# Optimization experiments

Measured on AMD Instinct MI355X. Metric: run time of the kernel, lower is better.

Reference implementation:

```python
import jax, jax.numpy as jnp
import numpy as np

K = 9            # connections per output pixel
GA = 2           # global additional samples
RA = 2           # relative additional samples
VS = 4 + GA + RA # 2^rank neighbours + sampled
REGION = 12      # int(0.25 * 48) per spatial dim
MMULT = 0.1
MIN_SIGMA = 0.05
SIGMA_SCALE = 0.05
SIGMA_BOOST = 2.0


def setup_inputs() -> dict:
    key = jax.random.key(0)
    ks = jax.random.split(key, 8)
    b, cin, h, w = 8, 128, 48, 48
    cout = 256
    hidden = cin * 4

    def lin_init(k, fan_out, fan_in):
        bound = 1.0 / np.sqrt(fan_in)
        kw, kb = jax.random.split(k)
        W = jax.random.uniform(kw, (fan_out, fan_in), minval=-bound, maxval=bound, dtype=jnp.float32)
        bb = jax.random.uniform(kb, (fan_out,), minval=-bound, maxval=bound, dtype=jnp.float32)
        return W, bb

    x = jax.random.normal(ks[0], (b, cin, h, w), dtype=jnp.float32)
    W1, b1 = lin_init(ks[1], hidden, 2)          # toparams layer 1 (adaptive=False -> 2 coord inputs)
    W2, b2 = lin_init(ks[2], 3 * K, hidden)      # toparams layer 2 -> k means (2d) + k sigmas
    Wu, bu = lin_init(ks[3], cout, K * cin)      # unify linear
    gints = jax.random.randint(ks[4], (b, h, w, K, GA, 2), 0, h, dtype=jnp.int32)      # global samples (h==w)
    roff = jax.random.randint(ks[5], (b, h, w, K, RA, 2), 0, REGION, dtype=jnp.int32)  # relative offsets
    return {"x": x, "W1": W1, "b1": b1, "W2": W2, "b2": b2, "Wu": Wu, "bu": bu,
            "gints": gints, "roff": roff}


def reference(x, W1, b1, W2, b2, Wu, bu, gints, roff):
    b, c, h, w = x.shape
    s = jnp.array([h, w], dtype=x.dtype)                       # spatial range per dim
    s_int = jnp.array([h, w], dtype=jnp.int32)

    # normalized coordinate grid in [0,1], (h, w, 2) with [.,.,0]=row, [.,.,1]=col
    rows = jnp.arange(h, dtype=x.dtype) / (h - 1)
    cols = jnp.arange(w, dtype=x.dtype) / (w - 1)
    coords = jnp.stack(jnp.meshgrid(rows, cols, indexing='ij'), axis=-1)

    # hypernetwork: per-pixel coords -> K 2d mean offsets + K sigmas
    inp = jnp.broadcast_to(coords, (b, h, w, 2))
    hid = jax.nn.relu(inp @ W1.T + b1)
    params = hid @ W2.T + b2                                   # (b,h,w,3K)
    means_raw = params[..., :2 * K].reshape(b, h, w, K, 2)
    sig_raw = params[..., 2 * K:]                              # (b,h,w,K)

    # mids: inverse of the sigmoid scaling applied to the pixel's own coordinate
    pix = coords * (s - 1)                                     # pixel coordinates
    sc = pix / (s - 1) * 0.9999 + 0.00005
    mids = jnp.log(sc / (1.0 - sc))                            # (h,w,2)

    # transform_means: sigmoid -> [0, s-1]
    means = jax.nn.sigmoid(mids[None, :, :, None, :] + MMULT * means_raw) * (s - 1)  # (b,h,w,K,2)
    # transform_sigmas: softplus(. + boost) + min, per-dim scale, then sigma_scale
    sigmas = (jax.nn.softplus(sig_raw + SIGMA_BOOST) + MIN_SIGMA)[..., None] * s * SIGMA_SCALE  # (b,h,w,K,2)

    # ---- integer index generation (non-differentiable) ----
    fl = jnp.floor(jax.lax.stop_gradient(means)).astype(jnp.int32)   # (b,h,w,K,2)
    combos = jnp.array([[0, 0], [0, 1], [1, 0], [1, 1]], dtype=jnp.int32)
    neigh = fl[..., None, :] + combos                                 # (b,h,w,K,4,2)
    rel = fl[..., None, :] + roff - REGION // 2                       # (b,h,w,K,RA,2)
    ints = jnp.concatenate([neigh, gints, rel], axis=-2) % s_int      # (b,h,w,K,VS,2)

    # duplicate masking: zero any tuple that occurred earlier along VS
    eq = jnp.all(ints[..., :, None, :] == ints[..., None, :, :], axis=-1)  # (...,VS,VS)
    lower = jnp.tril(jnp.ones((VS, VS), dtype=bool), k=-1)
    dups = jnp.any(eq & lower, axis=-1)                               # (b,h,w,K,VS)

    # unnormalized gaussian densities of integer points under (means, sigmas)
    diff = (ints.astype(x.dtype) - means[..., None, :]) / sigmas[..., None, :]
    props = jnp.exp(-0.5 * jnp.sum(diff * diff, axis=-1))             # (b,h,w,K,VS)
    props = jnp.where(dups, jnp.zeros((), x.dtype), props)
    weights = props / jnp.sum(props, axis=-1, keepdims=True)          # mvalues are all-ones

    # irregular gather of input channel vectors at sampled pixels
    lin = ints[..., 0] * w + ints[..., 1]                             # (b,h,w,K,VS)
    flat = x.transpose(0, 2, 3, 1).reshape(b, h * w, c)
    feats = flat[jnp.arange(b)[:, None], lin.reshape(b, -1)]          # (b, h*w*K*VS, c)
    feats = feats.reshape(b, h, w, K, VS, c)

    feats = jnp.einsum('bhwkvc,bhwkv->bhwkc', feats, weights)         # weighted reduce over VS
    feats = feats.reshape(b, h, w, K * c)
    out = feats @ Wu.T + bu                                           # unify linear
    return out.transpose(0, 3, 1, 2)                                  # (b, cout, h, w)
```

## Files before the change

### kernel.cpp

```cpp
#include <hip/hip_runtime.h>
#include <hip/hip_bf16.h>
#include <hip/hip_fp16.h>

#define BB 8
#define CIN 128
#define HH 48
#define WW 48
#define HW 2304
#define KK 9
#define COUT 256
#define KC 1152
#define MM 18432
#define MT 16
#define SFP 136

#define LIGHT_BARRIER() asm volatile("s_waitcnt lgkmcnt(0)\n\ts_barrier" ::: "memory")

typedef short bf16x8_t __attribute__((ext_vector_type(8)));
typedef float f32x4_t  __attribute__((ext_vector_type(4)));

static __device__ __forceinline__ float b2f(short u) {
    union { unsigned int i; float f; } c;
    c.i = ((unsigned int)(unsigned short)u) << 16;
    return c.f;
}

__global__ __launch_bounds__(256) void prep_kernel(
    const float* __restrict__ x, __hip_bfloat16* __restrict__ xT,
    const float* __restrict__ Wu, bf16x8_t* __restrict__ Bp,
    const float* __restrict__ W1, const float* __restrict__ b1,
    const float* __restrict__ W2, const float* __restrict__ b2,
    float* __restrict__ means, float* __restrict__ sigmas, int* __restrict__ fls)
{
    int bid = blockIdx.x;
    int t = threadIdx.x;

    if (bid < 576) {
        __shared__ float tile[64][65];
        int ij0 = (bid % 36) * 64;
        int c0  = ((bid / 36) % 2) * 64;
        int b   = bid / 72;
        int ijl = t & 63, cl = t >> 6;
        #pragma unroll
        for (int i = 0; i < 16; i++) {
            int cc = i*4 + cl;
            tile[cc][ijl] = x[(size_t)(b*CIN + c0 + cc) * HW + ij0 + ijl];
        }
        __syncthreads();
        int cl2 = t & 63, ijl2 = t >> 6;
        #pragma unroll
        for (int i = 0; i < 16; i++) {
            int ij = i*4 + ijl2;
            xT[(size_t)(b*HW + ij0 + ij) * CIN + c0 + cl2] = __float2bfloat16(tile[cl2][ij]);
        }
    } else if (bid < 720) {
        int idx = (bid - 576) * 256 + t;
        int lane = idx & 63;
        int rest = idx >> 6;
        int ksub = rest % 36, tile16 = rest / 36;
        const float* src = Wu + (size_t)(tile16*16 + (lane & 15)) * KC
                              + ksub*32 + (lane >> 4)*8;
        union { bf16x8_t v; __hip_bfloat16 h[8]; } o;
        #pragma unroll
        for (int j = 0; j < 8; j++) o.h[j] = __float2bfloat16(src[j]);
        Bp[idx] = o.v;
    } else {
        int wave = t >> 6, lane = t & 63;
        int p = (bid - 720) * 4 + wave;
        int iy = p / WW, ix = p % WW;
        float ryf = (float)iy / 47.0f;
        float rxf = (float)ix / 47.0f;
        double ry = (double)ryf, rx = (double)rxf;

        double h[8];
        #pragma unroll
        for (int jj = 0; jj < 8; jj++) {
            int j = lane*8 + jj;
            double v = ry * (double)W1[j*2+0] + rx * (double)W1[j*2+1] + (double)b1[j];
            h[jj] = v > 0.0 ? v : 0.0;
        }
        double par[27];
        #pragma unroll
        for (int o = 0; o < 27; o++) {
            const float4* w4 = (const float4*)(W2 + (size_t)o*512 + lane*8);
            float4 wa = w4[0], wb = w4[1];
            double s = (double)wa.x*h[0] + (double)wa.y*h[1]
                     + (double)wa.z*h[2] + (double)wa.w*h[3]
                     + (double)wb.x*h[4] + (double)wb.y*h[5]
                     + (double)wb.z*h[6] + (double)wb.w*h[7];
            par[o] = s;
        }
        #pragma unroll
        for (int o = 0; o < 27; o++) {
            #pragma unroll
            for (int d = 1; d < 64; d <<= 1)
                par[o] += __shfl_xor(par[o], d, 64);
            par[o] += (double)b2[o];
        }
        if (lane < KK) {
            int k = lane;
            double scy = ry * 0.9999 + 5e-05;
            double scx = rx * 0.9999 + 5e-05;
            double midy = log(scy / (1.0 - scy));
            double midx = log(scx / (1.0 - scx));
            double zy = midy + 0.1 * par[2*k+0];
            double zx = midx + 0.1 * par[2*k+1];
            double my = 47.0 / (1.0 + exp(-zy));
            double mx = 47.0 / (1.0 + exp(-zx));
            double sr = par[18 + k] + 2.0;
            double sp = (sr > 0.0 ? sr : 0.0) + log1p(exp(-fabs(sr)));
            double sg = (sp + 0.05) * 48.0 * 0.05;
            means[(p*KK + k)*2 + 0] = (float)my;
            means[(p*KK + k)*2 + 1] = (float)mx;
            sigmas[p*KK + k] = (float)sg;
            fls[(p*KK + k)*2 + 0] = (int)floor(my);
            fls[(p*KK + k)*2 + 1] = (int)floor(mx);
        }
    }
}

__global__ __launch_bounds__(256, 3) void fused_kernel(
    const float* __restrict__ means, const float* __restrict__ sigmas,
    const int* __restrict__ fls, const int* __restrict__ gints,
    const int* __restrict__ roff, const short* __restrict__ xT,
    const bf16x8_t* __restrict__ Bp, const float* __restrict__ bu,
    float* __restrict__ out)
{
    __shared__ unsigned int s_tap[KK*MT*8];
    __shared__ __align__(16) short s_feat[KK][MT*SFP];

    int t = threadIdx.x;
    int b   = blockIdx.x & 7;
    int grp = blockIdx.x >> 3;
    int ij0 = grp * MT;
    int m0  = b * HW + ij0;

    if (t < KK*MT) {
        int p = t;
        int k = p >> 4, row = p & 15;
        int ij = ij0 + row;
        int bij = m0 + row;
        int fy = fls[(ij*KK + k)*2 + 0];
        int fx = fls[(ij*KK + k)*2 + 1];
        float my = means[(ij*KK + k)*2 + 0];
        float mx = means[(ij*KK + k)*2 + 1];
        float sg = sigmas[ij*KK + k];
        int lins[8]; float ws[8];
        #pragma unroll
        for (int v = 0; v < 8; v++) {
            int iy, ix;
            if (v < 4) {
                iy = fy + (v >> 1); ix = fx + (v & 1);
            } else if (v < 6) {
                int base = ((bij*KK + k)*2 + (v - 4)) * 2;
                iy = gints[base]; ix = gints[base + 1];
            } else {
                int base = ((bij*KK + k)*2 + (v - 6)) * 2;
                iy = fy + roff[base] - 6; ix = fx + roff[base + 1] - 6;
            }
            iy = ((iy % HH) + HH) % HH;
            ix = ((ix % WW) + WW) % WW;
            lins[v] = iy * WW + ix;
            float dy = ((float)iy - my) / sg;
            float dx = ((float)ix - mx) / sg;
            ws[v] = expf(-0.5f * (dy*dy + dx*dx));
        }
        #pragma unroll
        for (int v = 1; v < 8; v++) {
            bool dup = false;
            #pragma unroll
            for (int u = 0; u < 8; u++) if (u < v) dup = dup || (lins[u] == lins[v]);
            if (dup) ws[v] = 0.0f;
        }
        float sum = 0.0f;
        #pragma unroll
        for (int v = 0; v < 8; v++) sum += ws[v];
        float inv = 1.0f / sum;
        #pragma unroll
        for (int v = 0; v < 8; v++) {
            unsigned short hb = __half_as_ushort(__float2half(ws[v] * inv));
            s_tap[p*8+v] = ((unsigned int)lins[v] << 16) | (unsigned int)hb;
        }
    }
    LIGHT_BARRIER();

    const short* xb = xT + (size_t)b * (HW * CIN);
    int lane = t & 63, wave = t >> 6;
    int grow = t >> 4, gc0 = (t & 15) << 3;
    int arow = lane & 15, aq = lane >> 4;

    {
        bf16x8_t tap[8];
        float    wgt[8];
        {
            const unsigned int* tp = &s_tap[(0*MT + grow)*8];
            #pragma unroll
            for (int v = 0; v < 8; v++) {
                unsigned int e = tp[v];
                wgt[v] = __half2float(__ushort_as_half((unsigned short)(e & 0xffffu)));
                tap[v] = *(const bf16x8_t*)(xb + (size_t)(e >> 16) * CIN + gc0);
            }
        }
        for (int k = 0; k < KK; k++) {
            float a0[8];
            #pragma unroll
            for (int j = 0; j < 8; j++) a0[j] = 0.0f;
            #pragma unroll
            for (int v = 0; v < 8; v++) {
                float w = wgt[v]; bf16x8_t d8 = tap[v];
                #pragma unroll
                for (int j = 0; j < 8; j++) a0[j] += w * b2f(d8[j]);
            }
            if (k < KK - 1) {
                const unsigned int* tp = &s_tap[((k+1)*MT + grow)*8];
                #pragma unroll
                for (int v = 0; v < 8; v++) {
                    unsigned int e = tp[v];
                    wgt[v] = __half2float(__ushort_as_half((unsigned short)(e & 0xffffu)));
                    tap[v] = *(const bf16x8_t*)(xb + (size_t)(e >> 16) * CIN + gc0);
                }
            }
            union { bf16x8_t v8; __hip_bfloat16 hh[8]; } o;
            #pragma unroll
            for (int j = 0; j < 8; j++) o.hh[j] = __float2bfloat16(a0[j]);
            *(bf16x8_t*)(&s_feat[k][grow*SFP + gc0]) = o.v8;
        }
    }
    LIGHT_BARRIER();
    f32x4_t acc[4] = {};
    for (int k = 0; k < KK; k++) {
        bf16x8_t Bf[16];
        {
            int base = (wave*4*36 + k*4)*64 + lane;
            #pragma unroll
            for (int tl = 0; tl < 4; tl++)
                #pragma unroll
                for (int s4 = 0; s4 < 4; s4++)
                    Bf[tl*4 + s4] = Bp[base + (tl*36 + s4)*64];
        }
        const short* fb = s_feat[k];
        bf16x8_t av[4];
        #pragma unroll
        for (int s4 = 0; s4 < 4; s4++)
            av[s4] = *(const bf16x8_t*)(fb + arow*SFP + s4*32 + aq*8);
        #pragma unroll
        for (int tl = 0; tl < 4; tl++)
            #pragma unroll
            for (int s4 = 0; s4 < 4; s4++)
                acc[tl] = __builtin_amdgcn_mfma_f32_16x16x32_bf16(av[s4], Bf[tl*4 + s4], acc[tl], 0, 0, 0);
    }

    #pragma unroll
    for (int tl = 0; tl < 4; tl++) {
        int n = (wave*4 + tl)*16 + arow;
        float bv = bu[n];
        f32x4_t vv;
        vv[0] = acc[tl][0] + bv;
        vv[1] = acc[tl][1] + bv;
        vv[2] = acc[tl][2] + bv;
        vv[3] = acc[tl][3] + bv;
        *(f32x4_t*)(out + ((size_t)b * COUT + n) * HW + ij0 + aq*4) = vv;
    }
}

extern "C" void kernel_launch(void* const* d_in, const int* in_sizes, int n_in,
                              void* d_out, int out_size, void* d_ws, size_t ws_size,
                              hipStream_t stream)
{
    const float* x   = (const float*)d_in[0];
    const float* W1  = (const float*)d_in[1];
    const float* b1  = (const float*)d_in[2];
    const float* W2  = (const float*)d_in[3];
    const float* b2  = (const float*)d_in[4];
    const float* Wu  = (const float*)d_in[5];
    const float* bu  = (const float*)d_in[6];
    const int* gints = (const int*)d_in[7];
    const int* roff  = (const int*)d_in[8];
    float* out = (float*)d_out;

    char* ws = (char*)d_ws;
    float* ws_means  = (float*)(ws + 0);
    float* ws_sigma  = (float*)(ws + 165888);
    int*   ws_fl     = (int*  )(ws + 248832);
    short* ws_xT     = (short*)(ws + 414720);
    bf16x8_t* ws_bp  = (bf16x8_t*)(ws + 5133312);

    prep_kernel<<<1296, 256, 0, stream>>>(x, (__hip_bfloat16*)ws_xT, Wu, ws_bp,
                                          W1, b1, W2, b2,
                                          ws_means, ws_sigma, ws_fl);
    fused_kernel<<<MM/MT, 256, 0, stream>>>(ws_means, ws_sigma, ws_fl, gints, roff,
                                            ws_xT, ws_bp, bu, out);
}
```

Baseline: 150.3 us.

## Split fused tap/gather/GEMM kernel into three separate kernels via global buffers

```diff
diff --git a/kernel.cpp b/kernel.cpp
--- a/kernel.cpp
+++ b/kernel.cpp
@@ -11,10 +11,7 @@
 #define COUT 256
 #define KC 1152
 #define MM 18432
-#define MT 16
-#define SFP 136
-
-#define LIGHT_BARRIER() asm volatile("s_waitcnt lgkmcnt(0)\n\ts_barrier" ::: "memory")
+#define EPI 20736
 
 typedef short bf16x8_t __attribute__((ext_vector_type(8)));
 typedef float f32x4_t  __attribute__((ext_vector_type(4)));
@@ -119,135 +116,122 @@
     }
 }
 
-__global__ __launch_bounds__(256, 3) void fused_kernel(
+__global__ __launch_bounds__(256) void taps_kernel(
     const float* __restrict__ means, const float* __restrict__ sigmas,
     const int* __restrict__ fls, const int* __restrict__ gints,
-    const int* __restrict__ roff, const short* __restrict__ xT,
-    const bf16x8_t* __restrict__ Bp, const float* __restrict__ bu,
-    float* __restrict__ out)
-{
-    __shared__ unsigned int s_tap[KK*MT*8];
-    __shared__ __align__(16) short s_feat[KK][MT*SFP];
-
+    const int* __restrict__ roff, unsigned int* __restrict__ tapout)
+{
+    int e = blockIdx.x * 256 + threadIdx.x;
+    int bij = e / KK, k = e - bij*KK;
+    int ij = bij % HW;
+
+    int fy = fls[(ij*KK + k)*2 + 0];
+    int fx = fls[(ij*KK + k)*2 + 1];
+    float my = means[(ij*KK + k)*2 + 0];
+    float mx = means[(ij*KK + k)*2 + 1];
+    float sg = sigmas[ij*KK + k];
+    int lins[8]; float ws[8];
+    #pragma unroll
+    for (int v = 0; v < 8; v++) {
+        int iy, ix;
+        if (v < 4) {
+            iy = fy + (v >> 1); ix = fx + (v & 1);
+        } else if (v < 6) {
+            int base = ((bij*KK + k)*2 + (v - 4)) * 2;
+            iy = gints[base]; ix = gints[base + 1];
+        } else {
+            int base = ((bij*KK + k)*2 + (v - 6)) * 2;
+            iy = fy + roff[base] - 6; ix = fx + roff[base + 1] - 6;
+        }
+        iy = ((iy % HH) + HH) % HH;
+        ix = ((ix % WW) + WW) % WW;
+        lins[v] = iy * WW + ix;
+        float dy = ((float)iy - my) / sg;
+        float dx = ((float)ix - mx) / sg;
+        ws[v] = expf(-0.5f * (dy*dy + dx*dx));
+    }
+    #pragma unroll
+    for (int v = 1; v < 8; v++) {
+        bool dup = false;
+        #pragma unroll
+        for (int u = 0; u < 8; u++) if (u < v) dup = dup || (lins[u] == lins[v]);
+        if (dup) ws[v] = 0.0f;
+    }
+    float sum = 0.0f;
+    #pragma unroll
+    for (int v = 0; v < 8; v++) sum += ws[v];
+    float inv = 1.0f / sum;
+    #pragma unroll
+    for (int v = 0; v < 8; v++) {
+        unsigned short hb = __half_as_ushort(__float2half(ws[v] * inv));
+        tapout[(size_t)e*8 + v] = ((unsigned int)lins[v] << 16) | (unsigned int)hb;
+    }
+}
+
+__global__ __launch_bounds__(256) void gather_kernel(
+    const unsigned int* __restrict__ taps, const short* __restrict__ xT,
+    short* __restrict__ feats)
+{
+    int t = threadIdx.x;
+    int img = blockIdx.x & 7;
+    int sub = blockIdx.x >> 3;
+    int e   = img*EPI + sub*16 + (t >> 4);
+    int gc0 = (t & 15) << 3;
+
+    int bij = e / KK, k = e - bij*KK;
+    const short* xb = xT + (size_t)img * (HW * CIN);
+    const unsigned int* tp = taps + (size_t)e*8;
+
+    bf16x8_t tap[8];
+    float    wgt[8];
+    #pragma unroll
+    for (int v = 0; v < 8; v++) {
+        unsigned int ee = tp[v];
+        wgt[v] = __half2float(__ushort_as_half((unsigned short)(ee & 0xffffu)));
+        tap[v] = *(const bf16x8_t*)(xb + (size_t)(ee >> 16) * CIN + gc0);
+    }
+    float a0[8];
+    #pragma unroll
+    for (int j = 0; j < 8; j++) a0[j] = 0.0f;
+    #pragma unroll
+    for (int v = 0; v < 8; v++) {
+        float w = wgt[v]; bf16x8_t d8 = tap[v];
+        #pragma unroll
+        for (int j = 0; j < 8; j++) a0[j] += w * b2f(d8[j]);
+    }
+    union { bf16x8_t v8; __hip_bfloat16 hh[8]; } o;
+    #pragma unroll
+    for (int j = 0; j < 8; j++) o.hh[j] = __float2bfloat16(a0[j]);
+    *(bf16x8_t*)(feats + (size_t)bij*KC + k*CIN + gc0) = o.v8;
+}
+
+__global__ __launch_bounds__(256) void gemm_kernel(
+    const short* __restrict__ feats, const bf16x8_t* __restrict__ Bp,
+    const float* __restrict__ bu, float* __restrict__ out)
+{
     int t = threadIdx.x;
     int b   = blockIdx.x & 7;
     int grp = blockIdx.x >> 3;
-    int ij0 = grp * MT;
-    int m0  = b * HW + ij0;
-
-    if (t < KK*MT) {
-        int p = t;
-        int k = p >> 4, row = p & 15;
-        int ij = ij0 + row;
-        int bij = m0 + row;
-        int fy = fls[(ij*KK + k)*2 + 0];
-        int fx = fls[(ij*KK + k)*2 + 1];
-        float my = means[(ij*KK + k)*2 + 0];
-        float mx = means[(ij*KK + k)*2 + 1];
-        float sg = sigmas[ij*KK + k];
-        int lins[8]; float ws[8];
-        #pragma unroll
-        for (int v = 0; v < 8; v++) {
-            int iy, ix;
-            if (v < 4) {
-                iy = fy + (v >> 1); ix = fx + (v & 1);
-            } else if (v < 6) {
-                int base = ((bij*KK + k)*2 + (v - 4)) * 2;
-                iy = gints[base]; ix = gints[base + 1];
-            } else {
-                int base = ((bij*KK + k)*2 + (v - 6)) * 2;
-                iy = fy + roff[base] - 6; ix = fx + roff[base + 1] - 6;
-            }
-            iy = ((iy % HH) + HH) % HH;
-            ix = ((ix % WW) + WW) % WW;
-            lins[v] = iy * WW + ix;
-            float dy = ((float)iy - my) / sg;
-            float dx = ((float)ix - mx) / sg;
-            ws[v] = expf(-0.5f * (dy*dy + dx*dx));
-        }
-        #pragma unroll
-        for (int v = 1; v < 8; v++) {
-            bool dup = false;
-            #pragma unroll
-            for (int u = 0; u < 8; u++) if (u < v) dup = dup || (lins[u] == lins[v]);
-            if (dup) ws[v] = 0.0f;
-        }
-        float sum = 0.0f;
-        #pragma unroll
-        for (int v = 0; v < 8; v++) sum += ws[v];
-        float inv = 1.0f / sum;
-        #pragma unroll
-        for (int v = 0; v < 8; v++) {
-            unsigned short hb = __half_as_ushort(__float2half(ws[v] * inv));
-            s_tap[p*8+v] = ((unsigned int)lins[v] << 16) | (unsigned int)hb;
-        }
-    }
-    LIGHT_BARRIER();
-
-    const short* xb = xT + (size_t)b * (HW * CIN);
+    int ij0 = grp * 16;
+    size_t pos0 = (size_t)b * HW + ij0;
+
     int lane = t & 63, wave = t >> 6;
-    int grow = t >> 4, gc0 = (t & 15) << 3;
     int arow = lane & 15, aq = lane >> 4;
 
-    {
-        bf16x8_t tap[8];
-        float    wgt[8];
-        {
-            const unsigned int* tp = &s_tap[(0*MT + grow)*8];
-            #pragma unroll
-            for (int v = 0; v < 8; v++) {
-                unsigned int e = tp[v];
-                wgt[v] = __half2float(__ushort_as_half((unsigned short)(e & 0xffffu)));
-                tap[v] = *(const bf16x8_t*)(xb + (size_t)(e >> 16) * CIN + gc0);
-            }
-        }
-        for (int k = 0; k < KK; k++) {
-            float a0[8];
-            #pragma unroll
-            for (int j = 0; j < 8; j++) a0[j] = 0.0f;
-            #pragma unroll
-            for (int v = 0; v < 8; v++) {
-                float w = wgt[v]; bf16x8_t d8 = tap[v];
-                #pragma unroll
-                for (int j = 0; j < 8; j++) a0[j] += w * b2f(d8[j]);
-            }
-            if (k < KK - 1) {
-                const unsigned int* tp = &s_tap[((k+1)*MT + grow)*8];
-                #pragma unroll
-                for (int v = 0; v < 8; v++) {
-                    unsigned int e = tp[v];
-                    wgt[v] = __half2float(__ushort_as_half((unsigned short)(e & 0xffffu)));
-                    tap[v] = *(const bf16x8_t*)(xb + (size_t)(e >> 16) * CIN + gc0);
-                }
-            }
-            union { bf16x8_t v8; __hip_bfloat16 hh[8]; } o;
-            #pragma unroll
-            for (int j = 0; j < 8; j++) o.hh[j] = __float2bfloat16(a0[j]);
-            *(bf16x8_t*)(&s_feat[k][grow*SFP + gc0]) = o.v8;
-        }
-    }
-    LIGHT_BARRIER();
+    const short* ap = feats + (pos0 + arow) * KC + aq*8;
     f32x4_t acc[4] = {};
+
     for (int k = 0; k < KK; k++) {
-        bf16x8_t Bf[16];
-        {
-            int base = (wave*4*36 + k*4)*64 + lane;
-            #pragma unroll
-            for (int tl = 0; tl < 4; tl++)
-                #pragma unroll
-                for (int s4 = 0; s4 < 4; s4++)
-                    Bf[tl*4 + s4] = Bp[base + (tl*36 + s4)*64];
-        }
-        const short* fb = s_feat[k];
         bf16x8_t av[4];
         #pragma unroll
         for (int s4 = 0; s4 < 4; s4++)
-            av[s4] = *(const bf16x8_t*)(fb + arow*SFP + s4*32 + aq*8);
+            av[s4] = *(const bf16x8_t*)(ap + k*CIN + s4*32);
+        int base = (wave*4*36 + k*4)*64 + lane;
         #pragma unroll
         for (int tl = 0; tl < 4; tl++)
             #pragma unroll
             for (int s4 = 0; s4 < 4; s4++)
-                acc[tl] = __builtin_amdgcn_mfma_f32_16x16x32_bf16(av[s4], Bf[tl*4 + s4], acc[tl], 0, 0, 0);
+                acc[tl] = __builtin_amdgcn_mfma_f32_16x16x32_bf16(av[s4], Bp[base + (tl*36 + s4)*64], acc[tl], 0, 0, 0);
     }
 
     #pragma unroll
@@ -284,10 +268,14 @@
     int*   ws_fl     = (int*  )(ws + 248832);
     short* ws_xT     = (short*)(ws + 414720);
     bf16x8_t* ws_bp  = (bf16x8_t*)(ws + 5133312);
+    unsigned int* ws_tap = (unsigned int*)(ws + 5723136);
+    short* ws_feats  = (short*)(ws + 11031552);
 
     prep_kernel<<<1296, 256, 0, stream>>>(x, (__hip_bfloat16*)ws_xT, Wu, ws_bp,
                                           W1, b1, W2, b2,
                                           ws_means, ws_sigma, ws_fl);
-    fused_kernel<<<MM/MT, 256, 0, stream>>>(ws_means, ws_sigma, ws_fl, gints, roff,
-                                            ws_xT, ws_bp, bu, out);
-}
+    taps_kernel<<<648, 256, 0, stream>>>(ws_means, ws_sigma, ws_fl, gints, roff,
+                                         ws_tap);
+    gather_kernel<<<10368, 256, 0, stream>>>(ws_tap, ws_xT, ws_feats);
+    gemm_kernel<<<1152, 256, 0, stream>>>(ws_feats, ws_bp, bu, out);
+}
```

Measured after the change: 177.5 us. 18.1% more time.
